# Kernel optimization log

Hardware: AMD Instinct MI355X
Metric: run time of the kernel (lower is better)

## Reference

```python
import jax, jax.numpy as jnp
import numpy as np

N_BITS = 8
LEVELS = 2 ** N_BITS - 1  # 255 quantization levels (asymmetric uniform)
EPS = 1e-8


def _round_ste(x):
    # straight-through round (forward: round, backward: identity)
    return x + jax.lax.stop_gradient(jnp.round(x) - x)


def _fake_quant_uniform(x):
    # dynamic per-tensor asymmetric uniform quantization (UniformQuantizer)
    xmin = jnp.min(x)
    xmax = jnp.max(x)
    scale = jnp.maximum((xmax - xmin) / LEVELS, EPS)
    zero_point = jnp.round(-xmin / scale)
    x_int = jnp.clip(_round_ste(x / scale) + zero_point, 0, LEVELS)
    return (x_int - zero_point) * scale


def setup_inputs() -> dict:
    key = jax.random.key(0)
    kA, kB = jax.random.split(key)
    A = jax.random.normal(kA, (4, 4096, 4096), dtype=jnp.float32)  # [batch, M, K]
    B = jax.random.normal(kB, (4096, 4096), dtype=jnp.float32)     # [K, N]
    return {"A": A, "B": B}


def reference(A, B):
    # QuantMatMul.forward with use_input_quant=True, use_weight_quant=True
    Aq = _fake_quant_uniform(A)
    Bq = _fake_quant_uniform(B)
    return Aq @ Bq  # [batch, M, N]
```

## Files before the change

### kernel.cpp

```cpp
#include <hip/hip_runtime.h>


#define K_DIM 4096
#define N_COLS 4096
#define M_ROWS 16384

typedef __attribute__((ext_vector_type(4))) int int4v;
typedef __attribute__((ext_vector_type(16))) int int16v;

static const size_t OFF_AQ = 0;
static const size_t OFF_BT = (size_t)64 << 20;
static const size_t OFF_RS = OFF_BT + ((size_t)16 << 20);
static const size_t OFF_CS = OFF_RS + (size_t)M_ROWS * 4;
static const size_t OFF_MM = OFF_CS + (size_t)N_COLS * 4;

__device__ __forceinline__ unsigned enc_f(float f) {
  unsigned u = __float_as_uint(f);
  return (u & 0x80000000u) ? ~u : (u | 0x80000000u);
}
__device__ __forceinline__ float dec_f(unsigned e) {
  unsigned u = (e & 0x80000000u) ? (e & 0x7fffffffu) : ~e;
  return __uint_as_float(u);
}

__device__ __forceinline__ int quantize1(float x, float r, float zp) {
  return (int)(fminf(fmaxf(rintf(x * r) + zp, 0.0f), 255.0f)) - 128;
}

__device__ __forceinline__ void gload16(const void* g, void* l) {
  __builtin_amdgcn_global_load_lds(
      (const __attribute__((address_space(1))) unsigned int*)g,
      (__attribute__((address_space(3))) unsigned int*)l, 16, 0, 0);
}

__device__ __forceinline__ void qparams_a(const unsigned* mm, float& ra, float& zpa) {
  const float amin = dec_f(mm[0]), amax = dec_f(mm[1]);
  const float sa = fmaxf((amax - amin) / 255.0f, 1e-8f);
  zpa = rintf(-amin / sa);
  ra = 1.0f / sa;
}
__device__ __forceinline__ void qparams_b(const unsigned* mm, float& rb, float& zpb) {
  const float bmin = dec_f(mm[2]), bmax = dec_f(mm[3]);
  const float sb = fmaxf((bmax - bmin) / 255.0f, 1e-8f);
  zpb = rintf(-bmin / sb);
  rb = 1.0f / sb;
}

__global__ void init_mm_k(unsigned* mm) {
  if (threadIdx.x == 0) {
    mm[0] = 0xFFFFFFFFu; mm[1] = 0u;
    mm[2] = 0xFFFFFFFFu; mm[3] = 0u;
  }
}

__global__ __launch_bounds__(256) void minmax_k(const float4* __restrict__ A,
                                                const float4* __restrict__ B,
                                                unsigned* __restrict__ mm) {
  const bool isB = blockIdx.x >= 4096;
  const float4* __restrict__ x = isB ? B : A;
  const long n4 = isB ? (long)K_DIM * N_COLS / 4 : (long)M_ROWS * K_DIM / 4;
  const int nblk = isB ? 1024 : 4096;
  const int bid = isB ? (int)blockIdx.x - 4096 : (int)blockIdx.x;
  unsigned* m = mm + (isB ? 2 : 0);

  float lo = 3.402823466e38f, hi = -3.402823466e38f;
  long i = (long)bid * blockDim.x + threadIdx.x;
  const long stride = (long)nblk * blockDim.x;
  for (; i < n4; i += stride) {
    float4 v = x[i];
    lo = fminf(lo, fminf(fminf(v.x, v.y), fminf(v.z, v.w)));
    hi = fmaxf(hi, fmaxf(fmaxf(v.x, v.y), fmaxf(v.z, v.w)));
  }
  for (int off = 32; off; off >>= 1) {
    lo = fminf(lo, __shfl_down(lo, off));
    hi = fmaxf(hi, __shfl_down(hi, off));
  }
  __shared__ float slo[4], shi[4];
  const int t = threadIdx.x;
  if ((t & 63) == 0) { slo[t >> 6] = lo; shi[t >> 6] = hi; }
  __syncthreads();
  if (t == 0) {
    for (int w = 1; w < 4; w++) { lo = fminf(lo, slo[w]); hi = fmaxf(hi, shi[w]); }
    atomicMin(&m[0], enc_f(lo));
    atomicMax(&m[1], enc_f(hi));
  }
}

__global__ __launch_bounds__(256) void quantA_k(const float* __restrict__ A,
                                                signed char* __restrict__ Aq,
                                                int* __restrict__ rowsum,
                                                const unsigned* __restrict__ mm) {
  float ra, zpa;
  qparams_a(mm, ra, zpa);
  const int row = blockIdx.x, t = threadIdx.x;
  const float4* src = (const float4*)(A + (size_t)row * K_DIM);
  unsigned* dst = (unsigned*)(Aq + (size_t)row * K_DIM);
  int sum = 0;
#pragma unroll
  for (int j = 0; j < 4; j++) {
    const int d = j * 256 + t;
    float4 v = src[d];
    int q0 = quantize1(v.x, ra, zpa);
    int q1 = quantize1(v.y, ra, zpa);
    int q2 = quantize1(v.z, ra, zpa);
    int q3 = quantize1(v.w, ra, zpa);
    sum += q0 + q1 + q2 + q3;
    dst[d] = ((unsigned)q0 & 255u) | (((unsigned)q1 & 255u) << 8) |
             (((unsigned)q2 & 255u) << 16) | (((unsigned)q3 & 255u) << 24);
  }
  for (int off = 32; off; off >>= 1) sum += __shfl_down(sum, off);
  __shared__ int sw[4];
  if ((t & 63) == 0) sw[t >> 6] = sum;
  __syncthreads();
  if (t == 0) rowsum[row] = sw[0] + sw[1] + sw[2] + sw[3];
}

__global__ __launch_bounds__(256) void quantB_k(const float* __restrict__ B,
                                                signed char* __restrict__ Bt,
                                                const unsigned* __restrict__ mm) {
  float rb, zpb;
  qparams_b(mm, rb, zpb);
  __shared__ unsigned char s[64][72];
  const int n0 = blockIdx.x * 64, k0 = blockIdx.y * 64;
  const int t = threadIdx.x;
  const int kr = t >> 2, tl = t & 3;
  const float* rowp = B + (size_t)(k0 + kr) * N_COLS + n0;
#pragma unroll
  for (int j = 0; j < 4; j++) {
    const int fi = tl + j * 4;
    float4 v = *(const float4*)(rowp + fi * 4);
    int q0 = quantize1(v.x, rb, zpb);
    int q1 = quantize1(v.y, rb, zpb);
    int q2 = quantize1(v.z, rb, zpb);
    int q3 = quantize1(v.w, rb, zpb);
    *(unsigned*)&s[kr][fi * 4] = ((unsigned)q0 & 255u) | (((unsigned)q1 & 255u) << 8) |
                                 (((unsigned)q2 & 255u) << 16) | (((unsigned)q3 & 255u) << 24);
  }
  __syncthreads();
  const int nr = t >> 2;
  const int kb = tl * 16;
  unsigned w[4];
#pragma unroll
  for (int jj = 0; jj < 4; jj++) {
    unsigned b0 = s[kb + jj * 4 + 0][nr];
    unsigned b1 = s[kb + jj * 4 + 1][nr];
    unsigned b2 = s[kb + jj * 4 + 2][nr];
    unsigned b3 = s[kb + jj * 4 + 3][nr];
    w[jj] = b0 | (b1 << 8) | (b2 << 16) | (b3 << 24);
  }
  int4v o = {(int)w[0], (int)w[1], (int)w[2], (int)w[3]};
  *(int4v*)(Bt + (size_t)(n0 + nr) * K_DIM + (k0 + kb)) = o;
}

__global__ __launch_bounds__(256) void colsum_k(const signed char* __restrict__ Bt,
                                                int* __restrict__ colsum) {
  const int n = blockIdx.x, t = threadIdx.x;
  const int4v v = ((const int4v*)(Bt + (size_t)n * K_DIM))[t];
  int sum = 0;
#pragma unroll
  for (int c = 0; c < 4; c++) {
    unsigned w = (unsigned)v[c];
    sum += (int)(signed char)(w & 255u) + (int)(signed char)((w >> 8) & 255u) +
           (int)(signed char)((w >> 16) & 255u) + (int)(signed char)((w >> 24) & 255u);
  }
  for (int off = 32; off; off >>= 1) sum += __shfl_down(sum, off);
  __shared__ int sw[4];
  if ((t & 63) == 0) sw[t >> 6] = sum;
  __syncthreads();
  if (t == 0) colsum[n] = sw[0] + sw[1] + sw[2] + sw[3];
}

__global__ __launch_bounds__(512, 4) void gemm_k(const signed char* __restrict__ Aq,
                                                 const signed char* __restrict__ Bt,
                                                 float* __restrict__ C,
                                                 const int* __restrict__ rowsum,
                                                 const int* __restrict__ colsum,
                                                 const unsigned* __restrict__ mm) {
  __shared__ signed char lds[49152];
  const int t = threadIdx.x;

  const int orig = blockIdx.x;
  const int wgid = (orig & 7) * 256 + (orig >> 3);
  const int m0 = (wgid >> 5) * 256;
  const int n0 = (wgid & 31) * 128;

  const int w = t >> 6, l = t & 63;
  const int wm = (w >> 2) * 128;
  const int wn = (w & 3) * 32;
  const int r32 = l & 31, h = l >> 5;
  const int u = r32 >> 2, c4 = (r32 & 3) * 4;

  unsigned aAddr[4][2], bAddr[2];
#pragma unroll
  for (int m = 0; m < 4; ++m)
#pragma unroll
    for (int kk = 0; kk < 2; ++kk)
      aAddr[m][kk] = (unsigned)(((wm + 32 * m) >> 2) + u) * 256 +
                     (unsigned)(((c4 + 2 * kk + h) ^ u) << 4);
#pragma unroll
  for (int kk = 0; kk < 2; ++kk)
    bAddr[kk] = 16384u + (unsigned)(8 * (w & 3) + u) * 256 +
                (unsigned)(((c4 + 2 * kk + h) ^ u) << 4);

  const int bs_ = t & 15, Rq = t >> 4;
  const int b16 = bs_ ^ (Rq & 7);
  const int sc = b16 >> 2, slb = b16 & 3;
  const signed char* pA0 = Aq + (size_t)(m0 + 4 * Rq + sc) * K_DIM + slb * 16;
  const signed char* pA1 = pA0 + (size_t)128 * K_DIM;
  const signed char* pB  = Bt + (size_t)(n0 + 4 * Rq + sc) * K_DIM + slb * 16;

  int16v acc[4] = {};

#define STAGE(NXT) do {                                   \
    gload16(pA0, lds + (NXT) + t * 16);                   \
    gload16(pA1, lds + (NXT) + 8192 + t * 16);            \
    gload16(pB,  lds + (NXT) + 16384 + t * 16);           \
    pA0 += 64; pA1 += 64; pB += 64; } while (0)

#define MFMA4(A0, A1, A2, A3, B0)                                            \
    __builtin_amdgcn_s_setprio(1);                                           \
    acc[0] = __builtin_amdgcn_mfma_i32_32x32x32_i8(A0, B0, acc[0], 0, 0, 0); \
    acc[1] = __builtin_amdgcn_mfma_i32_32x32x32_i8(A1, B0, acc[1], 0, 0, 0); \
    acc[2] = __builtin_amdgcn_mfma_i32_32x32x32_i8(A2, B0, acc[2], 0, 0, 0); \
    acc[3] = __builtin_amdgcn_mfma_i32_32x32x32_i8(A3, B0, acc[3], 0, 0, 0); \
    __builtin_amdgcn_s_setprio(0);

#define COMP(CUR) do {                                                \
    int4v b0 = *(const int4v*)(lds + (CUR) + bAddr[0]);               \
    int4v a0 = *(const int4v*)(lds + (CUR) + aAddr[0][0]);            \
    int4v a1 = *(const int4v*)(lds + (CUR) + aAddr[1][0]);            \
    int4v a2 = *(const int4v*)(lds + (CUR) + aAddr[2][0]);            \
    int4v a3 = *(const int4v*)(lds + (CUR) + aAddr[3][0]);            \
    MFMA4(a0, a1, a2, a3, b0)                                         \
    b0 = *(const int4v*)(lds + (CUR) + bAddr[1]);                     \
    a0 = *(const int4v*)(lds + (CUR) + aAddr[0][1]);                  \
    a1 = *(const int4v*)(lds + (CUR) + aAddr[1][1]);                  \
    a2 = *(const int4v*)(lds + (CUR) + aAddr[2][1]);                  \
    a3 = *(const int4v*)(lds + (CUR) + aAddr[3][1]);                  \
    MFMA4(a0, a1, a2, a3, b0)                                         \
  } while (0)

  STAGE(0);
  __syncthreads();

#pragma unroll 1
  for (int it = 0; it < 31; ++it) {
    STAGE(24576); COMP(0);     __syncthreads();
    STAGE(0);     COMP(24576); __syncthreads();
  }
  STAGE(24576); COMP(0); __syncthreads();
  COMP(24576);

#undef STAGE
#undef MFMA4
#undef COMP

  const float amin = dec_f(mm[0]), amax = dec_f(mm[1]);
  const float bmin = dec_f(mm[2]), bmax = dec_f(mm[3]);
  const float sa = fmaxf((amax - amin) / 255.0f, 1e-8f);
  const float sb = fmaxf((bmax - bmin) / 255.0f, 1e-8f);
  const int za = (int)rintf(-amin / sa) - 128;
  const int zb = (int)rintf(-bmin / sb) - 128;
  const float sab = sa * sb;
  const int kzz = K_DIM * za * zb;
  const int col = n0 + wn + r32;
  const int cs = za * colsum[col];
#pragma unroll
  for (int m = 0; m < 4; ++m) {
    const int rbase = m0 + wm + m * 32 + 4 * h;
#pragma unroll
    for (int r = 0; r < 16; ++r) {
      const int row = rbase + (r & 3) + 8 * (r >> 2);
      const int v = acc[m][r] - zb * rowsum[row] - cs + kzz;
      C[(size_t)row * N_COLS + col] = sab * (float)v;
    }
  }
}

extern "C" void kernel_launch(void* const* d_in, const int* in_sizes, int n_in,
                              void* d_out, int out_size, void* d_ws, size_t ws_size,
                              hipStream_t stream) {
  const float* A = (const float*)d_in[0];
  const float* B = (const float*)d_in[1];
  float* C = (float*)d_out;
  char* ws = (char*)d_ws;
  signed char* Aq = (signed char*)(ws + OFF_AQ);
  signed char* Bt = (signed char*)(ws + OFF_BT);
  int* rowsum = (int*)(ws + OFF_RS);
  int* colsum = (int*)(ws + OFF_CS);
  unsigned* mm = (unsigned*)(ws + OFF_MM);

  init_mm_k<<<1, 64, 0, stream>>>(mm);
  minmax_k<<<5120, 256, 0, stream>>>((const float4*)A, (const float4*)B, mm);
  quantA_k<<<M_ROWS, 256, 0, stream>>>(A, Aq, rowsum, mm);
  quantB_k<<<dim3(64, 64), 256, 0, stream>>>(B, Bt, mm);
  colsum_k<<<N_COLS, 256, 0, stream>>>(Bt, colsum);
  gemm_k<<<2048, 512, 0, stream>>>(Aq, Bt, C, rowsum, colsum, mm);
}
```

Before: 894.5 us.

## Triple-buffer int8 GEMM with vmcnt waits, 2x2 warp tiling, fuse colsum into quantB

The GEMM moves from a double-buffered LDS pipeline with __syncthreads to a triple-buffered one. Explicit s_waitcnt vmcnt and a raw barrier let two stages of loads stay in flight. Warp tiling changes from 4x1 MFMA tiles per warp to a 2x2 arrangement, which cuts LDS fragment reads per MFMA. The column-sum kernel is removed: sums are now computed inside quantB and accumulated with atomics into a buffer that the init kernel zeroes. The cost is larger LDS use (72KB), which may reduce occupancy, plus atomic contention.

After: 882.0 us. Within noise of the previous version (-1.4%).

```diff
diff --git a/kernel.cpp b/kernel.cpp
--- a/kernel.cpp
+++ b/kernel.cpp
@@ -46,8 +46,11 @@
   rb = 1.0f / sb;
 }
 
-__global__ void init_mm_k(unsigned* mm) {
-  if (threadIdx.x == 0) {
+__global__ __launch_bounds__(256) void init_k(unsigned* __restrict__ mm,
+                                              int* __restrict__ colsum) {
+  const int i = blockIdx.x * 256 + threadIdx.x;
+  if (i < N_COLS) colsum[i] = 0;
+  if (i == N_COLS) {
     mm[0] = 0xFFFFFFFFu; mm[1] = 0u;
     mm[2] = 0xFFFFFFFFu; mm[3] = 0u;
   }
@@ -117,6 +120,7 @@
 
 __global__ __launch_bounds__(256) void quantB_k(const float* __restrict__ B,
                                                 signed char* __restrict__ Bt,
+                                                int* __restrict__ colsum,
                                                 const unsigned* __restrict__ mm) {
   float rb, zpb;
   qparams_b(mm, rb, zpb);
@@ -140,6 +144,7 @@
   const int nr = t >> 2;
   const int kb = tl * 16;
   unsigned w[4];
+  int psum = 0;
 #pragma unroll
   for (int jj = 0; jj < 4; jj++) {
     unsigned b0 = s[kb + jj * 4 + 0][nr];
@@ -147,27 +152,14 @@
     unsigned b2 = s[kb + jj * 4 + 2][nr];
     unsigned b3 = s[kb + jj * 4 + 3][nr];
     w[jj] = b0 | (b1 << 8) | (b2 << 16) | (b3 << 24);
+    psum += (int)(signed char)b0 + (int)(signed char)b1 +
+            (int)(signed char)b2 + (int)(signed char)b3;
   }
   int4v o = {(int)w[0], (int)w[1], (int)w[2], (int)w[3]};
   *(int4v*)(Bt + (size_t)(n0 + nr) * K_DIM + (k0 + kb)) = o;
-}
-
-__global__ __launch_bounds__(256) void colsum_k(const signed char* __restrict__ Bt,
-                                                int* __restrict__ colsum) {
-  const int n = blockIdx.x, t = threadIdx.x;
-  const int4v v = ((const int4v*)(Bt + (size_t)n * K_DIM))[t];
-  int sum = 0;
-#pragma unroll
-  for (int c = 0; c < 4; c++) {
-    unsigned w = (unsigned)v[c];
-    sum += (int)(signed char)(w & 255u) + (int)(signed char)((w >> 8) & 255u) +
-           (int)(signed char)((w >> 16) & 255u) + (int)(signed char)((w >> 24) & 255u);
-  }
-  for (int off = 32; off; off >>= 1) sum += __shfl_down(sum, off);
-  __shared__ int sw[4];
-  if ((t & 63) == 0) sw[t >> 6] = sum;
-  __syncthreads();
-  if (t == 0) colsum[n] = sw[0] + sw[1] + sw[2] + sw[3];
+  psum += __shfl_xor(psum, 1);
+  psum += __shfl_xor(psum, 2);
+  if (tl == 0) atomicAdd(&colsum[n0 + nr], psum);
 }
 
 __global__ __launch_bounds__(512, 4) void gemm_k(const signed char* __restrict__ Aq,
@@ -176,7 +168,7 @@
                                                  const int* __restrict__ rowsum,
                                                  const int* __restrict__ colsum,
                                                  const unsigned* __restrict__ mm) {
-  __shared__ signed char lds[49152];
+  __shared__ signed char lds[73728];
   const int t = threadIdx.x;
 
   const int orig = blockIdx.x;
@@ -185,22 +177,24 @@
   const int n0 = (wgid & 31) * 128;
 
   const int w = t >> 6, l = t & 63;
-  const int wm = (w >> 2) * 128;
-  const int wn = (w & 3) * 32;
+  const int wm16 = (w >> 1) * 16;
+  const int wn16 = (w & 1) * 16;
   const int r32 = l & 31, h = l >> 5;
   const int u = r32 >> 2, c4 = (r32 & 3) * 4;
 
-  unsigned aAddr[4][2], bAddr[2];
-#pragma unroll
-  for (int m = 0; m < 4; ++m)
+  unsigned aAddr[2][2], bAddr[2][2];
+#pragma unroll
+  for (int mi = 0; mi < 2; ++mi)
 #pragma unroll
     for (int kk = 0; kk < 2; ++kk)
-      aAddr[m][kk] = (unsigned)(((wm + 32 * m) >> 2) + u) * 256 +
-                     (unsigned)(((c4 + 2 * kk + h) ^ u) << 4);
-#pragma unroll
-  for (int kk = 0; kk < 2; ++kk)
-    bAddr[kk] = 16384u + (unsigned)(8 * (w & 3) + u) * 256 +
-                (unsigned)(((c4 + 2 * kk + h) ^ u) << 4);
+      aAddr[mi][kk] = (unsigned)(wm16 + 8 * mi + u) * 256 +
+                      ((unsigned)((c4 + 2 * kk + h) ^ u) << 4);
+#pragma unroll
+  for (int ni = 0; ni < 2; ++ni)
+#pragma unroll
+    for (int kk = 0; kk < 2; ++kk)
+      bAddr[ni][kk] = 16384u + (unsigned)(wn16 + 8 * ni + u) * 256 +
+                      ((unsigned)((c4 + 2 * kk + h) ^ u) << 4);
 
   const int bs_ = t & 15, Rq = t >> 4;
   const int b16 = bs_ ^ (Rq & 7);
@@ -209,51 +203,61 @@
   const signed char* pA1 = pA0 + (size_t)128 * K_DIM;
   const signed char* pB  = Bt + (size_t)(n0 + 4 * Rq + sc) * K_DIM + slb * 16;
 
-  int16v acc[4] = {};
-
-#define STAGE(NXT) do {                                   \
-    gload16(pA0, lds + (NXT) + t * 16);                   \
-    gload16(pA1, lds + (NXT) + 8192 + t * 16);            \
-    gload16(pB,  lds + (NXT) + 16384 + t * 16);           \
+  int16v acc[2][2] = {};
+
+#define STAGE(SO) do {                                    \
+    gload16(pA0, lds + (SO) + t * 16);                    \
+    gload16(pA1, lds + (SO) + 8192 + t * 16);             \
+    gload16(pB,  lds + (SO) + 16384 + t * 16);            \
     pA0 += 64; pA1 += 64; pB += 64; } while (0)
 
-#define MFMA4(A0, A1, A2, A3, B0)                                            \
-    __builtin_amdgcn_s_setprio(1);                                           \
-    acc[0] = __builtin_amdgcn_mfma_i32_32x32x32_i8(A0, B0, acc[0], 0, 0, 0); \
-    acc[1] = __builtin_amdgcn_mfma_i32_32x32x32_i8(A1, B0, acc[1], 0, 0, 0); \
-    acc[2] = __builtin_amdgcn_mfma_i32_32x32x32_i8(A2, B0, acc[2], 0, 0, 0); \
-    acc[3] = __builtin_amdgcn_mfma_i32_32x32x32_i8(A3, B0, acc[3], 0, 0, 0); \
-    __builtin_amdgcn_s_setprio(0);
-
-#define COMP(CUR) do {                                                \
-    int4v b0 = *(const int4v*)(lds + (CUR) + bAddr[0]);               \
-    int4v a0 = *(const int4v*)(lds + (CUR) + aAddr[0][0]);            \
-    int4v a1 = *(const int4v*)(lds + (CUR) + aAddr[1][0]);            \
-    int4v a2 = *(const int4v*)(lds + (CUR) + aAddr[2][0]);            \
-    int4v a3 = *(const int4v*)(lds + (CUR) + aAddr[3][0]);            \
-    MFMA4(a0, a1, a2, a3, b0)                                         \
-    b0 = *(const int4v*)(lds + (CUR) + bAddr[1]);                     \
-    a0 = *(const int4v*)(lds + (CUR) + aAddr[0][1]);                  \
-    a1 = *(const int4v*)(lds + (CUR) + aAddr[1][1]);                  \
-    a2 = *(const int4v*)(lds + (CUR) + aAddr[2][1]);                  \
-    a3 = *(const int4v*)(lds + (CUR) + aAddr[3][1]);                  \
-    MFMA4(a0, a1, a2, a3, b0)                                         \
+#define MM_(A, B, CC) CC = __builtin_amdgcn_mfma_i32_32x32x32_i8(A, B, CC, 0, 0, 0)
+
+#define COMP(SO) do {                                                 \
+    int4v b0 = *(const int4v*)(lds + (SO) + bAddr[0][0]);             \
+    int4v b1 = *(const int4v*)(lds + (SO) + bAddr[1][0]);             \
+    int4v a0 = *(const int4v*)(lds + (SO) + aAddr[0][0]);             \
+    int4v a1 = *(const int4v*)(lds + (SO) + aAddr[1][0]);             \
+    __builtin_amdgcn_s_setprio(1);                                    \
+    MM_(a0, b0, acc[0][0]); MM_(a0, b1, acc[0][1]);                   \
+    MM_(a1, b0, acc[1][0]); MM_(a1, b1, acc[1][1]);                   \
+    __builtin_amdgcn_s_setprio(0);                                    \
+    b0 = *(const int4v*)(lds + (SO) + bAddr[0][1]);                   \
+    b1 = *(const int4v*)(lds + (SO) + bAddr[1][1]);                   \
+    a0 = *(const int4v*)(lds + (SO) + aAddr[0][1]);                   \
+    a1 = *(const int4v*)(lds + (SO) + aAddr[1][1]);                   \
+    __builtin_amdgcn_s_setprio(1);                                    \
+    MM_(a0, b0, acc[0][0]); MM_(a0, b1, acc[0][1]);                   \
+    MM_(a1, b0, acc[1][0]); MM_(a1, b1, acc[1][1]);                   \
+    __builtin_amdgcn_s_setprio(0);                                    \
   } while (0)
 
+#define WAITN(N) asm volatile("s_waitcnt vmcnt(" #N ")" ::: "memory")
+#define BARR do { __builtin_amdgcn_s_barrier();                       \
+                  __builtin_amdgcn_sched_barrier(0); } while (0)
+
+#define ITER(SC, SN) do { WAITN(3); BARR; STAGE(SN); COMP(SC); } while (0)
+
   STAGE(0);
-  __syncthreads();
+  STAGE(24576);
 
 #pragma unroll 1
-  for (int it = 0; it < 31; ++it) {
-    STAGE(24576); COMP(0);     __syncthreads();
-    STAGE(0);     COMP(24576); __syncthreads();
-  }
-  STAGE(24576); COMP(0); __syncthreads();
-  COMP(24576);
+  for (int g = 0; g < 20; ++g) {
+    ITER(0, 49152);
+    ITER(24576, 0);
+    ITER(49152, 24576);
+  }
+  ITER(0, 49152);
+  ITER(24576, 0);
+  WAITN(3); BARR; COMP(49152);
+  WAITN(0); BARR; COMP(0);
 
 #undef STAGE
-#undef MFMA4
+#undef MM_
 #undef COMP
+#undef WAITN
+#undef BARR
+#undef ITER
 
   const float amin = dec_f(mm[0]), amax = dec_f(mm[1]);
   const float bmin = dec_f(mm[2]), bmax = dec_f(mm[3]);
@@ -263,16 +267,19 @@
   const int zb = (int)rintf(-bmin / sb) - 128;
   const float sab = sa * sb;
   const int kzz = K_DIM * za * zb;
-  const int col = n0 + wn + r32;
-  const int cs = za * colsum[col];
-#pragma unroll
-  for (int m = 0; m < 4; ++m) {
-    const int rbase = m0 + wm + m * 32 + 4 * h;
+  const int wm = wm16 * 4, wn = wn16 * 4;
+  const int col0 = n0 + wn + r32;
+  const int cs0 = za * colsum[col0];
+  const int cs1 = za * colsum[col0 + 32];
+#pragma unroll
+  for (int mi = 0; mi < 2; ++mi) {
+    const int rbase = m0 + wm + mi * 32 + 4 * h;
 #pragma unroll
     for (int r = 0; r < 16; ++r) {
       const int row = rbase + (r & 3) + 8 * (r >> 2);
-      const int v = acc[m][r] - zb * rowsum[row] - cs + kzz;
-      C[(size_t)row * N_COLS + col] = sab * (float)v;
+      const int base = kzz - zb * rowsum[row];
+      C[(size_t)row * N_COLS + col0]      = sab * (float)(acc[mi][0][r] + base - cs0);
+      C[(size_t)row * N_COLS + col0 + 32] = sab * (float)(acc[mi][1][r] + base - cs1);
     }
   }
 }
@@ -290,10 +297,9 @@
   int* colsum = (int*)(ws + OFF_CS);
   unsigned* mm = (unsigned*)(ws + OFF_MM);
 
-  init_mm_k<<<1, 64, 0, stream>>>(mm);
+  init_k<<<17, 256, 0, stream>>>(mm, colsum);
   minmax_k<<<5120, 256, 0, stream>>>((const float4*)A, (const float4*)B, mm);
   quantA_k<<<M_ROWS, 256, 0, stream>>>(A, Aq, rowsum, mm);
-  quantB_k<<<dim3(64, 64), 256, 0, stream>>>(B, Bt, mm);
-  colsum_k<<<N_COLS, 256, 0, stream>>>(Bt, colsum);
+  quantB_k<<<dim3(64, 64), 256, 0, stream>>>(B, Bt, colsum, mm);
   gemm_k<<<2048, 512, 0, stream>>>(Aq, Bt, C, rowsum, colsum, mm);
 }
```
